# Optimization experiments

Measured on AMD Instinct MI355X. Metric: run time of the kernel, lower is better.

## Reference

```python
import jax, jax.numpy as jnp
import numpy as np

MGC_SIZE = 80
COND_DIM = 256
LSTM_SIZE = 500
UP_SCALE = 64  # prod([4,4,4])
TEMPERATURE = 1.0
EPS_MIN = -7.0


def setup_inputs() -> dict:
    key = jax.random.key(0)
    ks = jax.random.split(key, 10)
    B, T_FRAMES = 16, 32
    T = T_FRAMES * UP_SCALE  # 2048 decode steps
    s = 0.02  # weight scale for numerical stability (logvar goes through exp)
    return {
        "mgc": jax.random.normal(ks[0], (B, T_FRAMES, MGC_SIZE), dtype=jnp.float32),
        "eps": jax.random.normal(ks[1], (B, T), dtype=jnp.float32),
        # UpsampleNet stand-in: linear projection mgc_size->256, then repeat x64 in time
        "W_up": jax.random.normal(ks[2], (MGC_SIZE, COND_DIM), dtype=jnp.float32) * s,
        "b_up": jnp.zeros((COND_DIM,), dtype=jnp.float32),
        # LSTM (PyTorch layout, gate order i,f,g,o)
        "W_ih": jax.random.normal(ks[3], (4 * LSTM_SIZE, COND_DIM + 1), dtype=jnp.float32) * s,
        "W_hh": jax.random.normal(ks[4], (4 * LSTM_SIZE, LSTM_SIZE), dtype=jnp.float32) * s,
        "b_ih": jax.random.normal(ks[5], (4 * LSTM_SIZE,), dtype=jnp.float32) * s,
        "b_hh": jax.random.normal(ks[6], (4 * LSTM_SIZE,), dtype=jnp.float32) * s,
        # output Linear(lstm_size, 2)
        "W_out": jax.random.normal(ks[7], (2, LSTM_SIZE), dtype=jnp.float32) * s,
        "b_out": jnp.zeros((2,), dtype=jnp.float32),
    }


def reference(mgc, eps, W_up, b_up, W_ih, W_hh, b_ih, b_hh, W_out, b_out):
    B = mgc.shape[0]
    # conditioning: (B, T_frames, 80) -> (B, T, 256)
    cond = jnp.repeat(mgc @ W_up + b_up, UP_SCALE, axis=1)
    bias = b_ih + b_hh

    def step(carry, xs):
        h, c, x_prev = carry              # (B,H), (B,H), (B,)
        cond_t, eps_t = xs                # (B,256), (B,)
        inp = jnp.concatenate([cond_t, x_prev[:, None]], axis=1)  # (B,257)
        gates = inp @ W_ih.T + h @ W_hh.T + bias                  # (B,4H)
        i, f, g, o = jnp.split(gates, 4, axis=1)
        i = jax.nn.sigmoid(i)
        f = jax.nn.sigmoid(f)
        g = jnp.tanh(g)
        o = jax.nn.sigmoid(o)
        c = f * c + i * g
        h = o * jnp.tanh(c)
        out = h @ W_out.T + b_out         # (B,2)
        mean = jnp.tanh(out[:, 0])
        logvar = jnp.maximum(out[:, 1], EPS_MIN)  # clamp(min=eps_min)
        zz = mean + (eps_t * TEMPERATURE) * jnp.exp(logvar)
        return (h, c, zz), (mean, logvar, zz)

    h0 = jnp.zeros((B, LSTM_SIZE), dtype=mgc.dtype)
    c0 = jnp.zeros((B, LSTM_SIZE), dtype=mgc.dtype)
    x0 = jnp.zeros((B,), dtype=mgc.dtype)
    xs = (cond.transpose(1, 0, 2), eps.T)  # time-major
    _, (mean, logvar, zz) = jax.lax.scan(step, (h0, c0, x0), xs)
    # back to (B, T)
    return mean.T, logvar.T, zz.T
```

## Files before the change

kernel.cpp:

```cpp
#include <hip/hip_runtime.h>
#include <stdint.h>

#define TSTEPS 2048
#define NB     16
#define HDIM   500
#define NSLICE 16
#define NTHR   256
#define NBLK   256
#define GSTR   20
#define HSTR   264

#define HBASE(P) ((size_t)(P) * 4096)
#define DONE64   8192

typedef __attribute__((ext_vector_type(8))) short s16x8;
typedef __attribute__((ext_vector_type(4))) float f32x4;
typedef __attribute__((ext_vector_type(4))) unsigned int u32x4;

__device__ __forceinline__ unsigned short f2bf(float f) {
    unsigned u = __float_as_uint(f);
    u += 0x7FFFu + ((u >> 16) & 1u);
    return (unsigned short)(u >> 16);
}
__device__ __forceinline__ float bf2f(uint32_t hw) { return __uint_as_float(hw << 16); }
__device__ __forceinline__ float sigm(float x)   { return __fdividef(1.f, 1.f + __expf(-x)); }
__device__ __forceinline__ float tanhf_(float x) { return 1.f - __fdividef(2.f, __expf(2.f * x) + 1.f); }

__global__ void zero_ws_kernel(uint32_t* p, int n) {
    int i = blockIdx.x * blockDim.x + threadIdx.x;
    if (i < n) p[i] = 0u;
}

__global__ __launch_bounds__(NTHR, 1) void wavernn_persist(
    const float* __restrict__ mgc,  const float* __restrict__ eps,
    const float* __restrict__ Wup,  const float* __restrict__ bup,
    const float* __restrict__ Wih,  const float* __restrict__ Whh,
    const float* __restrict__ bih,  const float* __restrict__ bhh,
    const float* __restrict__ Wout, const float* __restrict__ bout,
    float* __restrict__ out, uint64_t* __restrict__ hb)
{
    if (blockIdx.x >= NSLICE) {
        const uint64_t* done = hb + DONE64;
        float a = (float)threadIdx.x * 1e-3f + (float)blockIdx.x;
        while (__hip_atomic_load(done, __ATOMIC_RELAXED,
                                 __HIP_MEMORY_SCOPE_AGENT) == 0ull) {
            #pragma unroll 16
            for (int i = 0; i < 4096; ++i) a = __builtin_fmaf(a, 1.0000001f, 1e-7f);
        }
        asm volatile("" :: "v"(a));
        return;
    }

    const int s    = blockIdx.x;
    const int tid  = threadIdx.x;
    const int lane = tid & 63;
    const int wave = tid >> 6;
    const int l16  = lane & 15;
    const int g    = lane >> 4;

    __shared__ __align__(16) uint32_t h_l[16 * HSTR];
    __shared__ __align__(16) float gates_l[NB * 132];
    __shared__ __align__(16) float gcond[128 * GSTR];
    __shared__ __align__(16) float condT[256 * NB];
    __shared__ __align__(16) float mgcl[NB * 80];
    __shared__ __align__(16) float eps_l[128 * NB];
    __shared__ __align__(16) float zz_l[NB];
    __shared__ __align__(16) uint64_t pub_l[256];
    __shared__ __align__(16) uint32_t part_l[16 * 17];
    __shared__ __align__(16) float stage_m[1024];
    __shared__ __align__(16) float stage_v[1024];
    __shared__ __align__(16) float stage_z[1024];

    s16x8 bfr[2][16];
    float wihl[2];
    #pragma unroll
    for (int t2 = 0; t2 < 2; ++t2) {
        const int q    = t2 * 16 + l16;
        const int hidx = s * 32 + q;
        const bool valid = hidx < HDIM;
        const int grow = wave * HDIM + hidx;
        wihl[t2] = valid ? Wih[grow * 257 + 256] : 0.f;
        #pragma unroll
        for (int kk = 0; kk < 16; ++kk) {
            const int k0 = kk * 32 + g * 8;
            s16x8 r;
            #pragma unroll
            for (int j = 0; j < 8; ++j) {
                const int k = k0 + j;
                const float v = (valid && k < HDIM) ? Whh[grow * HDIM + k] : 0.f;
                r[j] = (short)f2bf(v);
            }
            bfr[t2][kk] = r;
        }
    }
    const int b_e = tid >> 4;
    const int qh  = tid & 15;
    const int q0  = 2 * qh, q1 = q0 + 1;
    const int k0g = s * 32 + q0, k1g = s * 32 + q1;
    const float w0q0 = (k0g < HDIM) ? Wout[k0g]        : 0.f;
    const float w0q1 = (k1g < HDIM) ? Wout[k1g]        : 0.f;
    const float w1q0 = (k0g < HDIM) ? Wout[HDIM + k0g] : 0.f;
    const float w1q1 = (k1g < HDIM) ? Wout[HDIM + k1g] : 0.f;
    const float bout0 = bout[0], bout1 = bout[1];
    float cst0 = 0.f, cst1 = 0.f;

    auto rebuild = [&](int f) {
        for (int i = tid; i < NB * 80; i += NTHR) {
            const int b = i / 80, m = i - b * 80;
            mgcl[i] = mgc[(b * 32 + f) * 80 + m];
        }
        for (int i = tid; i < 64 * NB; i += NTHR) {
            const int st = i >> 4, b = i & 15;
            eps_l[((f & 1) * 64 + st) * NB + b] = eps[b * 2048 + f * 64 + st];
        }
        __syncthreads();
        {
            const int c = tid;
            float a[NB];
            #pragma unroll
            for (int b = 0; b < NB; ++b) a[b] = bup[c];
            for (int m = 0; m < 80; ++m) {
                const float w = Wup[m * 256 + c];
                #pragma unroll
                for (int b = 0; b < NB; ++b) a[b] += mgcl[b * 80 + m] * w;
            }
            #pragma unroll
            for (int b = 0; b < NB; ++b) condT[c * NB + b] = a[b];
        }
        __syncthreads();
        {
            const int n = tid >> 1, kc = tid & 1;
            const int gate = n >> 5, q = n & 31;
            const int hidx = s * 32 + q;
            const bool valid = hidx < HDIM;
            const int grow = gate * HDIM + hidx;
            float a[NB];
            #pragma unroll
            for (int b = 0; b < NB; ++b) a[b] = 0.f;
            if (valid) {
                const float* wr = Wih + (size_t)grow * 257 + kc * 128;
                for (int k = 0; k < 128; ++k) {
                    const float w = wr[k];
                    const float* cp = &condT[(kc * 128 + k) * NB];
                    #pragma unroll
                    for (int b = 0; b < NB; ++b) a[b] += cp[b] * w;
                }
            }
            if (kc == 0) {
                const float bias = valid ? (bih[grow] + bhh[grow]) : 0.f;
                #pragma unroll
                for (int b = 0; b < NB; ++b) gcond[n * GSTR + b] = a[b] + bias;
            }
            __syncthreads();
            if (kc == 1) {
                #pragma unroll
                for (int b = 0; b < NB; ++b) gcond[n * GSTR + b] += a[b];
            }
        }
        __syncthreads();
    };

    for (int i = tid; i < 16 * HSTR; i += NTHR) h_l[i] = 0u;
    rebuild(0);

    for (int t = 0; t <= TSTEPS; ++t) {
        if (t == TSTEPS && s != 0) break;

        if (t > 0 && tid < 128) {
            const int i = tid;
            const int p = i >> 3;
            const uint32_t want8 = (uint32_t)t & 0xFFu;
            uint64_t v[32];
            if (p == s) {
                const int lb = 32 * (i & 7);
                #pragma unroll
                for (int k = 0; k < 32; ++k) v[k] = pub_l[lb + k];
            } else {
                u32x4 u[16];
                const uint32_t* src = (const uint32_t*)(hb + HBASE((t & 1) ^ 1)
                                                        + (size_t)(2 * i) * 16);
                int guard = 0;
                while (true) {
                    #pragma unroll
                    for (int k = 0; k < 16; ++k)
                        asm volatile("global_load_dwordx4 %0, %1, off sc0 sc1"
                                     : "=v"(u[k]) : "v"(src + k * 4));
                    asm volatile("s_waitcnt vmcnt(0)" ::: "memory");
                    __builtin_amdgcn_sched_barrier(0);
                    bool ok = true;
                    #pragma unroll
                    for (int k = 0; k < 16; ++k)
                        ok &= ((u[k][1] & 0xFFu) == want8) & ((u[k][3] & 0xFFu) == want8);
                    if (ok || ++guard > (1 << 18)) break;
                    __builtin_amdgcn_s_sleep(1);
                }
                #pragma unroll
                for (int k = 0; k < 16; ++k) {
                    v[2 * k]     = (uint64_t)u[k][0] | ((uint64_t)u[k][1] << 32);
                    v[2 * k + 1] = (uint64_t)u[k][2] | ((uint64_t)u[k][3] << 32);
                }
            }
            #pragma unroll
            for (int rr = 0; rr < 2; ++rr) {
                const int b = (2 * i + rr) & 15;
                const uint64_t* rv = v + rr * 16;
                #pragma unroll
                for (int c = 0; c < 4; ++c) {
                    u32x4 w;
                    w[0] = (uint32_t)rv[4 * c];     w[1] = (uint32_t)rv[4 * c + 1];
                    w[2] = (uint32_t)rv[4 * c + 2]; w[3] = (uint32_t)rv[4 * c + 3];
                    *(u32x4*)&h_l[p * HSTR + (c * 16 + b) * 4] = w;
                }
                part_l[p * 17 + b] = (uint32_t)((rv[0] >> 40) & 0xFFFFu)
                                   | ((uint32_t)((rv[1] >> 40) & 0xFFFFu) << 16);
            }
        }
        __syncthreads();

        if (t > 0) {
            float o0[4], o1[4];
            #pragma unroll
            for (int j = 0; j < 4; ++j) {
                const uint32_t pp = part_l[l16 * 17 + (g * 4 + j)];
                o0[j] = bf2f(pp & 0xFFFFu);
                o1[j] = bf2f(pp >> 16);
            }
            #pragma unroll
            for (int m = 1; m < 16; m <<= 1) {
                #pragma unroll
                for (int j = 0; j < 4; ++j) {
                    o0[j] += __shfl_xor(o0[j], m);
                    o1[j] += __shfl_xor(o1[j], m);
                }
            }
            const int row = (t - 1) & 127;
            const int r64 = (t - 1) & 63;
            #pragma unroll
            for (int j = 0; j < 4; ++j) {
                const int B = g * 4 + j;
                const float mean = tanhf_(o0[j] + bout0);
                const float lv   = fmaxf(o1[j] + bout1, -7.f);
                const float zzv  = mean + eps_l[row * NB + B] * __expf(lv);
                if (l16 == 0) {
                    zz_l[B] = zzv;
                    if (s == 0) {
                        stage_m[r64 * 16 + B] = mean;
                        stage_v[r64 * 16 + B] = lv;
                        stage_z[r64 * 16 + B] = zzv;
                    }
                }
            }
            __builtin_amdgcn_sched_barrier(0);
        }

        if (t == TSTEPS) {
            __syncthreads();
            for (int k = tid; k < 1024; k += NTHR) {
                const int r = k >> 4, b = k & 15;
                out[         b * 2048 + 31 * 64 + r] = stage_m[k];
                out[32768 +  b * 2048 + 31 * 64 + r] = stage_v[k];
                out[65536 +  b * 2048 + 31 * 64 + r] = stage_z[k];
            }
            if (tid == 0)
                __hip_atomic_store(hb + DONE64, 1ull,
                                   __ATOMIC_RELAXED, __HIP_MEMORY_SCOPE_AGENT);
            break;
        }

        const int n0 = wave * 32 + l16;
        f32x4 acc0a = *(const f32x4*)&gcond[n0 * GSTR + g * 4];
        f32x4 acc1a = *(const f32x4*)&gcond[(n0 + 16) * GSTR + g * 4];
        f32x4 acc0b = {0.f, 0.f, 0.f, 0.f};
        f32x4 acc1b = {0.f, 0.f, 0.f, 0.f};
        s16x8 hfr[16];
        #pragma unroll
        for (int p = 0; p < 16; ++p)
            hfr[p] = *(const s16x8*)&h_l[p * HSTR + lane * 4];
        #pragma unroll
        for (int kk = 0; kk < 8; ++kk) {
            acc0a = __builtin_amdgcn_mfma_f32_16x16x32_bf16(hfr[kk],     bfr[0][kk],     acc0a, 0, 0, 0);
            acc1a = __builtin_amdgcn_mfma_f32_16x16x32_bf16(hfr[kk],     bfr[1][kk],     acc1a, 0, 0, 0);
            acc0b = __builtin_amdgcn_mfma_f32_16x16x32_bf16(hfr[kk + 8], bfr[0][kk + 8], acc0b, 0, 0, 0);
            acc1b = __builtin_amdgcn_mfma_f32_16x16x32_bf16(hfr[kk + 8], bfr[1][kk + 8], acc1b, 0, 0, 0);
        }

        f32x4 r0 = acc0a + acc0b;
        f32x4 r1 = acc1a + acc1b;
        if (t > 0) {
            const f32x4 zzq = *(const f32x4*)&zz_l[g * 4];
            r0 += zzq * wihl[0];
            r1 += zzq * wihl[1];
        }
        #pragma unroll
        for (int v = 0; v < 4; ++v) {
            gates_l[(g * 4 + v) * 132 + n0]      = r0[v];
            gates_l[(g * 4 + v) * 132 + n0 + 16] = r1[v];
        }
        __syncthreads();

        {
            const uint64_t tagb = ((uint64_t)(uint32_t)((t + 1) & 0xFF)) << 32;
            float po0, po1;
            uint32_t hp = 0;
            {
                const float gi = gates_l[b_e * 132 +      q0];
                const float gf = gates_l[b_e * 132 + 32 + q0];
                const float gg = gates_l[b_e * 132 + 64 + q0];
                const float go = gates_l[b_e * 132 + 96 + q0];
                cst0 = sigm(gf) * cst0 + sigm(gi) * tanhf_(gg);
                const float h = sigm(go) * tanhf_(cst0);
                if (k0g < HDIM) hp |= (uint32_t)f2bf(h);
                po0 = h * w0q0; po1 = h * w1q0;
            }
            {
                const float gi = gates_l[b_e * 132 +      q1];
                const float gf = gates_l[b_e * 132 + 32 + q1];
                const float gg = gates_l[b_e * 132 + 64 + q1];
                const float go = gates_l[b_e * 132 + 96 + q1];
                cst1 = sigm(gf) * cst1 + sigm(gi) * tanhf_(gg);
                const float h = sigm(go) * tanhf_(cst1);
                if (k1g < HDIM) hp |= ((uint32_t)f2bf(h)) << 16;
                po0 += h * w0q1; po1 += h * w1q1;
            }
            po0 += __shfl_xor(po0, 1);  po1 += __shfl_xor(po1, 1);
            po0 += __shfl_xor(po0, 2);  po1 += __shfl_xor(po1, 2);
            po0 += __shfl_xor(po0, 4);  po1 += __shfl_xor(po1, 4);
            po0 += __shfl_xor(po0, 8);  po1 += __shfl_xor(po1, 8);
            uint64_t rec = (uint64_t)hp | tagb;
            if (qh == 0) rec |= ((uint64_t)f2bf(po0)) << 40;
            if (qh == 1) rec |= ((uint64_t)f2bf(po1)) << 40;
            pub_l[b_e * 16 + qh] = rec;
        }
        __syncthreads();

        if (tid >= 128) {
            const int i = tid - 128;
            const u32x4 val = *(const u32x4*)&pub_l[2 * i];
            const uint64_t* gdst = hb + HBASE(t & 1) + (size_t)s * 256 + 2 * i;
            asm volatile("global_store_dwordx4 %0, %1, off sc0 sc1"
                         :: "v"(gdst), "v"(val) : "memory");
        }

        if (s == 0 && t > 0 && (t & 63) == 0 && tid >= 128) {
            const int fo = (t >> 6) - 1;
            for (int k = tid - 128; k < 1024; k += 128) {
                const int r = k >> 4, b = k & 15;
                out[         b * 2048 + fo * 64 + r] = stage_m[k];
                out[32768 +  b * 2048 + fo * 64 + r] = stage_v[k];
                out[65536 +  b * 2048 + fo * 64 + r] = stage_z[k];
            }
        }
        if (((t + 1) & 63) == 0 && (t + 1) < TSTEPS) rebuild((t + 1) >> 6);
    }
}

extern "C" void kernel_launch(void* const* d_in, const int* in_sizes, int n_in,
                              void* d_out, int out_size, void* d_ws, size_t ws_size,
                              hipStream_t stream) {
    const float* mgc  = (const float*)d_in[0];
    const float* eps  = (const float*)d_in[1];
    const float* Wup  = (const float*)d_in[2];
    const float* bup  = (const float*)d_in[3];
    const float* Wih  = (const float*)d_in[4];
    const float* Whh  = (const float*)d_in[5];
    const float* bih  = (const float*)d_in[6];
    const float* bhh  = (const float*)d_in[7];
    const float* Wout = (const float*)d_in[8];
    const float* bout = (const float*)d_in[9];

    uint64_t* hb = (uint64_t*)d_ws;

    zero_ws_kernel<<<65, 256, 0, stream>>>((uint32_t*)hb, 16386);
    wavernn_persist<<<NBLK, NTHR, 0, stream>>>(mgc, eps, Wup, bup, Wih, Whh,
                                               bih, bhh, Wout, bout,
                                               (float*)d_out, hb);
}
```

Measured before the change: 11.13 ms.

## Publish hidden state per-thread with atomic stores and widen poll to all threads

Each thread now writes its own packed hidden-state record straight to global memory with a relaxed atomic store, which removes the shared staging buffer and one block barrier per step. All 256 threads then poll and consume the exchange buffer, with a 12-bit step tag and the output partial sums carried as full fp32 split across lanes instead of bf16. The spinning filler blocks get an iteration cap, and the exchange poll sleeps only after a few retries. The risk is more global-memory polling traffic and possible visibility ordering issues from relaxed per-lane stores.

```diff
diff --git a/kernel.cpp b/kernel.cpp
--- a/kernel.cpp
+++ b/kernel.cpp
@@ -12,6 +12,7 @@
 
 #define HBASE(P) ((size_t)(P) * 4096)
 #define DONE64   8192
+#define ELECT64  8193
 
 typedef __attribute__((ext_vector_type(8))) short s16x8;
 typedef __attribute__((ext_vector_type(4))) float f32x4;
@@ -22,7 +23,6 @@
     u += 0x7FFFu + ((u >> 16) & 1u);
     return (unsigned short)(u >> 16);
 }
-__device__ __forceinline__ float bf2f(uint32_t hw) { return __uint_as_float(hw << 16); }
 __device__ __forceinline__ float sigm(float x)   { return __fdividef(1.f, 1.f + __expf(-x)); }
 __device__ __forceinline__ float tanhf_(float x) { return 1.f - __fdividef(2.f, __expf(2.f * x) + 1.f); }
 
@@ -42,8 +42,9 @@
     if (blockIdx.x >= NSLICE) {
         const uint64_t* done = hb + DONE64;
         float a = (float)threadIdx.x * 1e-3f + (float)blockIdx.x;
-        while (__hip_atomic_load(done, __ATOMIC_RELAXED,
-                                 __HIP_MEMORY_SCOPE_AGENT) == 0ull) {
+        for (int it = 0; it < 100000; ++it) {
+            if (__hip_atomic_load(done, __ATOMIC_RELAXED,
+                                  __HIP_MEMORY_SCOPE_AGENT) != 0ull) break;
             #pragma unroll 16
             for (int i = 0; i < 4096; ++i) a = __builtin_fmaf(a, 1.0000001f, 1e-7f);
         }
@@ -65,8 +66,8 @@
     __shared__ __align__(16) float mgcl[NB * 80];
     __shared__ __align__(16) float eps_l[128 * NB];
     __shared__ __align__(16) float zz_l[NB];
-    __shared__ __align__(16) uint64_t pub_l[256];
-    __shared__ __align__(16) uint32_t part_l[16 * 17];
+    __shared__ __align__(16) uint32_t part0_l[16 * 17];
+    __shared__ __align__(16) uint32_t part1_l[16 * 17];
     __shared__ __align__(16) float stage_m[1024];
     __shared__ __align__(16) float stage_v[1024];
     __shared__ __align__(16) float stage_z[1024];
@@ -163,57 +164,42 @@
     for (int i = tid; i < 16 * HSTR; i += NTHR) h_l[i] = 0u;
     rebuild(0);
 
+    const int gp = tid >> 4, gb = tid & 15;
+
     for (int t = 0; t <= TSTEPS; ++t) {
         if (t == TSTEPS && s != 0) break;
 
-        if (t > 0 && tid < 128) {
-            const int i = tid;
-            const int p = i >> 3;
-            const uint32_t want8 = (uint32_t)t & 0xFFu;
-            uint64_t v[32];
-            if (p == s) {
-                const int lb = 32 * (i & 7);
-                #pragma unroll
-                for (int k = 0; k < 32; ++k) v[k] = pub_l[lb + k];
-            } else {
-                u32x4 u[16];
-                const uint32_t* src = (const uint32_t*)(hb + HBASE((t & 1) ^ 1)
-                                                        + (size_t)(2 * i) * 16);
-                int guard = 0;
-                while (true) {
-                    #pragma unroll
-                    for (int k = 0; k < 16; ++k)
-                        asm volatile("global_load_dwordx4 %0, %1, off sc0 sc1"
-                                     : "=v"(u[k]) : "v"(src + k * 4));
-                    asm volatile("s_waitcnt vmcnt(0)" ::: "memory");
-                    __builtin_amdgcn_sched_barrier(0);
-                    bool ok = true;
-                    #pragma unroll
-                    for (int k = 0; k < 16; ++k)
-                        ok &= ((u[k][1] & 0xFFu) == want8) & ((u[k][3] & 0xFFu) == want8);
-                    if (ok || ++guard > (1 << 18)) break;
-                    __builtin_amdgcn_s_sleep(1);
-                }
-                #pragma unroll
-                for (int k = 0; k < 16; ++k) {
-                    v[2 * k]     = (uint64_t)u[k][0] | ((uint64_t)u[k][1] << 32);
-                    v[2 * k + 1] = (uint64_t)u[k][2] | ((uint64_t)u[k][3] << 32);
-                }
-            }
-            #pragma unroll
-            for (int rr = 0; rr < 2; ++rr) {
-                const int b = (2 * i + rr) & 15;
-                const uint64_t* rv = v + rr * 16;
-                #pragma unroll
-                for (int c = 0; c < 4; ++c) {
-                    u32x4 w;
-                    w[0] = (uint32_t)rv[4 * c];     w[1] = (uint32_t)rv[4 * c + 1];
-                    w[2] = (uint32_t)rv[4 * c + 2]; w[3] = (uint32_t)rv[4 * c + 3];
-                    *(u32x4*)&h_l[p * HSTR + (c * 16 + b) * 4] = w;
-                }
-                part_l[p * 17 + b] = (uint32_t)((rv[0] >> 40) & 0xFFFFu)
-                                   | ((uint32_t)((rv[1] >> 40) & 0xFFFFu) << 16);
-            }
+        if (t > 0) {
+            const uint32_t* src = (const uint32_t*)(hb + HBASE((t & 1) ^ 1)
+                                                    + (size_t)(gp * 16 + gb) * 16);
+            const uint32_t want12 = (uint32_t)t & 0xFFFu;
+            u32x4 u[8];
+            int guard = 0;
+            while (true) {
+                #pragma unroll
+                for (int i = 0; i < 8; ++i)
+                    asm volatile("global_load_dwordx4 %0, %1, off sc0 sc1"
+                                 : "=v"(u[i]) : "v"(src + i * 4));
+                asm volatile("s_waitcnt vmcnt(0)" ::: "memory");
+                __builtin_amdgcn_sched_barrier(0);
+                bool ok = true;
+                #pragma unroll
+                for (int i = 0; i < 8; ++i)
+                    ok &= ((u[i][1] & 0xFFFu) == want12) & ((u[i][3] & 0xFFFu) == want12);
+                if (ok || ++guard > (1 << 14)) break;
+                if (guard > 4) __builtin_amdgcn_s_sleep(1);
+            }
+            #pragma unroll
+            for (int c = 0; c < 4; ++c) {
+                u32x4 w;
+                w[0] = u[2 * c][0];     w[1] = u[2 * c][2];
+                w[2] = u[2 * c + 1][0]; w[3] = u[2 * c + 1][2];
+                *(u32x4*)&h_l[gp * HSTR + (c * 16 + gb) * 4] = w;
+            }
+            part0_l[gp * 17 + gb] = ((u[0][1] >> 12) & 0xFFFFu)
+                                  | (((u[0][3] >> 12) & 0xFFFFu) << 16);
+            part1_l[gp * 17 + gb] = ((u[1][1] >> 12) & 0xFFFFu)
+                                  | (((u[1][3] >> 12) & 0xFFFFu) << 16);
         }
         __syncthreads();
 
@@ -221,9 +207,8 @@
             float o0[4], o1[4];
             #pragma unroll
             for (int j = 0; j < 4; ++j) {
-                const uint32_t pp = part_l[l16 * 17 + (g * 4 + j)];
-                o0[j] = bf2f(pp & 0xFFFFu);
-                o1[j] = bf2f(pp >> 16);
+                o0[j] = __uint_as_float(part0_l[l16 * 17 + (g * 4 + j)]);
+                o1[j] = __uint_as_float(part1_l[l16 * 17 + (g * 4 + j)]);
             }
             #pragma unroll
             for (int m = 1; m < 16; m <<= 1) {
@@ -283,7 +268,6 @@
             acc0b = __builtin_amdgcn_mfma_f32_16x16x32_bf16(hfr[kk + 8], bfr[0][kk + 8], acc0b, 0, 0, 0);
             acc1b = __builtin_amdgcn_mfma_f32_16x16x32_bf16(hfr[kk + 8], bfr[1][kk + 8], acc1b, 0, 0, 0);
         }
-
         f32x4 r0 = acc0a + acc0b;
         f32x4 r1 = acc1a + acc1b;
         if (t > 0) {
@@ -299,7 +283,7 @@
         __syncthreads();
 
         {
-            const uint64_t tagb = ((uint64_t)(uint32_t)((t + 1) & 0xFF)) << 32;
+            const uint32_t tag12 = (uint32_t)(t + 1) & 0xFFFu;
             float po0, po1;
             uint32_t hp = 0;
             {
@@ -326,24 +310,20 @@
             po0 += __shfl_xor(po0, 2);  po1 += __shfl_xor(po1, 2);
             po0 += __shfl_xor(po0, 4);  po1 += __shfl_xor(po1, 4);
             po0 += __shfl_xor(po0, 8);  po1 += __shfl_xor(po1, 8);
-            uint64_t rec = (uint64_t)hp | tagb;
-            if (qh == 0) rec |= ((uint64_t)f2bf(po0)) << 40;
-            if (qh == 1) rec |= ((uint64_t)f2bf(po1)) << 40;
-            pub_l[b_e * 16 + qh] = rec;
-        }
-        __syncthreads();
-
-        if (tid >= 128) {
-            const int i = tid - 128;
-            const u32x4 val = *(const u32x4*)&pub_l[2 * i];
-            const uint64_t* gdst = hb + HBASE(t & 1) + (size_t)s * 256 + 2 * i;
-            asm volatile("global_store_dwordx4 %0, %1, off sc0 sc1"
-                         :: "v"(gdst), "v"(val) : "memory");
-        }
-
-        if (s == 0 && t > 0 && (t & 63) == 0 && tid >= 128) {
+            uint32_t piece = 0;
+            if (qh < 4) {
+                const uint32_t pb = (qh < 2) ? __float_as_uint(po0) : __float_as_uint(po1);
+                piece = (pb >> ((qh & 1) * 16)) & 0xFFFFu;
+            }
+            const uint64_t rec = (uint64_t)hp | ((uint64_t)tag12 << 32)
+                               | ((uint64_t)piece << 44);
+            __hip_atomic_store(hb + HBASE(t & 1) + ((size_t)(s * 16 + b_e) * 16 + qh),
+                               rec, __ATOMIC_RELAXED, __HIP_MEMORY_SCOPE_AGENT);
+        }
+
+        if (s == 0 && t > 0 && (t & 63) == 0) {
             const int fo = (t >> 6) - 1;
-            for (int k = tid - 128; k < 1024; k += 128) {
+            for (int k = tid; k < 1024; k += NTHR) {
                 const int r = k >> 4, b = k & 15;
                 out[         b * 2048 + fo * 64 + r] = stage_m[k];
                 out[32768 +  b * 2048 + fo * 64 + r] = stage_v[k];
@@ -370,7 +350,7 @@
 
     uint64_t* hb = (uint64_t*)d_ws;
 
-    zero_ws_kernel<<<65, 256, 0, stream>>>((uint32_t*)hb, 16386);
+    zero_ws_kernel<<<65, 256, 0, stream>>>((uint32_t*)hb, 16388);
     wavernn_persist<<<NBLK, NTHR, 0, stream>>>(mgc, eps, Wup, bup, Wih, Whh,
                                                bih, bhh, Wout, bout,
                                                (float*)d_out, hb);
```

Result: faster. 9.166 ms (-17.6%).
